# Kernel optimization log

Hardware: AMD Instinct MI355X
Metric: run time of the kernel (lower is better)

The kernel has to match this reference:

```python
import jax, jax.numpy as jnp
import numpy as np

HT_H, HT_W = 512, 512          # Hough accumulator grid
SPHERE_SIZE = 32768            # Gaussian-sphere bins
NUM_VOTES = 1_500_000          # rows in vote_mapping
BATCH, CHANNEL = 2, 64         # channel % 4 == 0 required by the module


def setup_inputs() -> dict:
    key = jax.random.key(0)
    k1, k2, k3, k4 = jax.random.split(key, 4)
    x = jax.random.normal(k1, (BATCH, CHANNEL, HT_H, HT_W), dtype=jnp.float32)
    ht_idx = jax.random.randint(k2, (NUM_VOTES,), 0, HT_H * HT_W, dtype=jnp.int32)
    sphere_idx = jax.random.randint(k3, (NUM_VOTES,), 0, SPHERE_SIZE, dtype=jnp.int32)
    weight = jax.random.uniform(k4, (NUM_VOTES,), dtype=jnp.float32)
    return {"x": x, "ht_idx": ht_idx, "sphere_idx": sphere_idx, "weight": weight}


def reference(x, ht_idx, sphere_idx, weight):
    b, c, h, w = x.shape
    # SPHERE_CUDA.forward: split channels into 4 groups, flatten HT grid
    xf = x.reshape(b * 4, c // 4, h * w)              # [B4, C4, HW]
    # HT2SPHERE: gather each vote's HT cell, scale by vote weight,
    # scatter-add into its sphere bin.
    votes = xf[:, :, ht_idx] * weight                  # [B4, C4, V]
    out = jax.ops.segment_sum(
        jnp.moveaxis(votes, -1, 0), sphere_idx, num_segments=SPHERE_SIZE
    )                                                  # [S, B4, C4]
    out = jnp.moveaxis(out, 0, -1)                     # [B4, C4, S]
    return out.reshape(b, c, SPHERE_SIZE)              # [B, C, S]
```

## Files before the change

### kernel.cpp

```cpp
#include <hip/hip_runtime.h>
#include <stdint.h>


#define S_BINS   32768
#define NBUCKET  1024
#define BINS     32
#define CAP      2048
#define CHUNK    4096
#define HT_BITS  18

__device__ __forceinline__ unsigned bf16_rne(float f) {
    unsigned u = __float_as_uint(f);
    return (u + 0x7FFFu + ((u >> 16) & 1u)) >> 16;
}

__global__ void transpose_x_bf16_kernel(const float* __restrict__ x,
                                        uint32_t* __restrict__ xTb, int HW) {
    __shared__ float tile[64][129];
    const int ht0 = blockIdx.x * 64;
    const int tid = threadIdx.x;
    for (int e = tid; e < 128 * 64; e += 256) {
        const int ch = e >> 6, hl = e & 63;
        tile[hl][ch] = x[(size_t)ch * HW + ht0 + hl];
    }
    __syncthreads();
    for (int e = tid; e < 64 * 64; e += 256) {
        const int hl = e >> 6, cp = e & 63;
        const unsigned lo = bf16_rne(tile[hl][cp]);
        const unsigned hi = bf16_rne(tile[hl][cp + 64]);
        xTb[(size_t)(ht0 + hl) * 64 + cp] = lo | (hi << 16);
    }
}

__global__ void init_kernel(int* __restrict__ cursor, int* __restrict__ spillCnt) {
    const int t = threadIdx.x;
    cursor[t] = t * CAP;
    if (t == 0) *spillCnt = 0;
}

__global__ __launch_bounds__(512) void reorder_kernel(
    const int* __restrict__ ht, const int* __restrict__ sp,
    const float* __restrict__ w, int* __restrict__ cursor,
    uint2* __restrict__ records, uint2* __restrict__ spillRec,
    int* __restrict__ spillBkt, int* __restrict__ spillCnt, int V) {
    __shared__ uint2 rec[CHUNK];
    __shared__ uint16_t bid[CHUNK];
    __shared__ int hist[NBUCKET], start[NBUCKET], cur[NBUCKET], gbase[NBUCKET];
    __shared__ int psum[512];
    const int blk = blockIdx.x, t = threadIdx.x;
    const int base = blk * CHUNK, end = min(V, base + CHUNK), n = end - base;
    hist[2 * t] = 0; hist[2 * t + 1] = 0;
    __syncthreads();
    for (int v = base + t; v < end; v += 512) atomicAdd(&hist[sp[v] >> 5], 1);
    __syncthreads();
    const int l0 = hist[2 * t], l1 = hist[2 * t + 1];
    psum[t] = l0 + l1;
    __syncthreads();
    for (int off = 1; off < 512; off <<= 1) {
        const int add = (t >= off) ? psum[t - off] : 0;
        __syncthreads();
        psum[t] += add;
        __syncthreads();
    }
    int run = (t == 0) ? 0 : psum[t - 1];
    start[2 * t]     = run; cur[2 * t]     = run; run += l0;
    start[2 * t + 1] = run; cur[2 * t + 1] = run;
    if (l0) gbase[2 * t]     = atomicAdd(&cursor[2 * t],     l0);
    if (l1) gbase[2 * t + 1] = atomicAdd(&cursor[2 * t + 1], l1);
    __syncthreads();
    for (int v = base + t; v < end; v += 512) {
        const int s = sp[v];
        const int b = s >> 5, sl = s & 31;
        const int pos = atomicAdd(&cur[b], 1);
        rec[pos] = make_uint2((unsigned)ht[v] | ((unsigned)sl << HT_BITS),
                              __float_as_uint(w[v]));
        bid[pos] = (uint16_t)b;
    }
    __syncthreads();
    for (int i = t; i < n; i += 512) {
        const int b = bid[i];
        const int slot = gbase[b] + (i - start[b]);
        if (slot < (b + 1) * CAP) {
            records[slot] = rec[i];
        } else {
            const int pos = atomicAdd(spillCnt, 1);
            spillRec[pos] = rec[i];
            spillBkt[pos] = b;
        }
    }
}

__global__ __launch_bounds__(512) void accum_kernel(
    const uint32_t* __restrict__ xTb, const uint2* __restrict__ records,
    const int* __restrict__ cursor, float* __restrict__ out) {
    __shared__ uint2 sorted[CAP];
    __shared__ __align__(16) char rawbuf[BINS * 129 * 4];
    __shared__ int hist[BINS], off[BINS + 1], cur[BINS];
    uint2* raw = (uint2*)rawbuf;
    const uint2* xTb2 = (const uint2*)xTb;
    const int bkt = blockIdx.x, t = threadIdx.x;
    const int lane = t & 63, wv = t >> 6;
    const int half = lane >> 5, hl = lane & 31;
    const int n = min(cursor[bkt] - bkt * CAP, CAP);
    const int rbase = bkt * CAP;
    float a[4][4];
#pragma unroll
    for (int i = 0; i < 4; ++i)
#pragma unroll
        for (int j = 0; j < 4; ++j) a[i][j] = 0.f;

    if (t < BINS) hist[t] = 0;
    __syncthreads();
    for (int i = t; i < n; i += 512) {
        const uint2 r = records[rbase + i];
        raw[i] = r;
        atomicAdd(&hist[(r.x >> HT_BITS) & 31], 1);
    }
    __syncthreads();
    if (t == 0) {
        int run = 0;
        for (int j = 0; j < BINS; ++j) { off[j] = run; cur[j] = run; run += hist[j]; }
        off[BINS] = run;
    }
    __syncthreads();
    for (int i = t; i < n; i += 512) {
        const uint2 r = raw[i];
        const int pos = atomicAdd(&cur[(r.x >> HT_BITS) & 31], 1);
        sorted[pos] = r;
    }
    __syncthreads();
#pragma unroll
    for (int bb = 0; bb < 4; ++bb) {
        const int f = wv * 4 + bb;
        const int s0 = off[f], s1 = off[f + 1];
        for (int k = s0; k < s1; k += 16) {
#pragma unroll
            for (int u = 0; u < 8; ++u) {
                const int kk = k + 2 * u + half;
                if (kk < s1) {
                    const uint2 r = sorted[kk];
                    const uint2 g = xTb2[(size_t)(r.x & 0x3FFFF) * 32 + hl];
                    const float wt = __uint_as_float(r.y);
                    a[bb][0] += __uint_as_float(g.x << 16) * wt;
                    a[bb][1] += __uint_as_float(g.x & 0xFFFF0000u) * wt;
                    a[bb][2] += __uint_as_float(g.y << 16) * wt;
                    a[bb][3] += __uint_as_float(g.y & 0xFFFF0000u) * wt;
                }
            }
        }
    }
#pragma unroll
    for (int bb = 0; bb < 4; ++bb)
#pragma unroll
        for (int j = 0; j < 4; ++j)
            a[bb][j] += __shfl_xor(a[bb][j], 32);
    __syncthreads();
    float* epi = (float*)rawbuf;
    if (half == 0) {
#pragma unroll
        for (int bb = 0; bb < 4; ++bb) {
            const int f = wv * 4 + bb;
            epi[f * 129 + 2 * hl]      = a[bb][0];
            epi[f * 129 + 2 * hl + 64] = a[bb][1];
            epi[f * 129 + 2 * hl + 1]  = a[bb][2];
            epi[f * 129 + 2 * hl + 65] = a[bb][3];
        }
    }
    __syncthreads();
    for (int i = t; i < 128 * BINS; i += 512) {
        const int ch = i >> 5, bin = i & 31;
        out[(size_t)ch * S_BINS + bkt * BINS + bin] = epi[bin * 129 + ch];
    }
}

__global__ void spill_kernel(const uint32_t* __restrict__ xTb,
                             const uint2* __restrict__ spillRec,
                             const int* __restrict__ spillBkt,
                             const int* __restrict__ spillCnt,
                             float* __restrict__ out) {
    const int cnt = *spillCnt;
    const long total = (long)cnt * 64;
    for (long u = (long)blockIdx.x * blockDim.x + threadIdx.x; u < total;
         u += (long)gridDim.x * blockDim.x) {
        const int i  = (int)(u >> 6);
        const int cp = (int)(u & 63);
        const uint2 r = spillRec[i];
        const int s = (spillBkt[i] << 5) | ((r.x >> HT_BITS) & 31);
        const uint32_t g = xTb[(size_t)(r.x & 0x3FFFF) * 64 + cp];
        const float wt = __uint_as_float(r.y);
        atomicAdd(&out[(size_t)cp * S_BINS + s],
                  __uint_as_float(g << 16) * wt);
        atomicAdd(&out[(size_t)(cp + 64) * S_BINS + s],
                  __uint_as_float(g & 0xFFFF0000u) * wt);
    }
}

__global__ void direct_kernel(const float* __restrict__ x,
                              const int* __restrict__ ht_idx,
                              const int* __restrict__ sp_idx,
                              const float* __restrict__ weight,
                              float* __restrict__ out, int V, int HW, int S,
                              int CH) {
    const int v = blockIdx.x * 2 + (threadIdx.x >> 7);
    if (v >= V) return;
    const int ch = threadIdx.x & 127;
    if (ch >= CH) return;
    atomicAdd(&out[(size_t)ch * S + sp_idx[v]],
              x[(size_t)ch * HW + ht_idx[v]] * weight[v]);
}

extern "C" void kernel_launch(void* const* d_in, const int* in_sizes, int n_in,
                              void* d_out, int out_size, void* d_ws, size_t ws_size,
                              hipStream_t stream) {
    const float* x  = (const float*)d_in[0];
    const int*   ht = (const int*)d_in[1];
    const int*   sp = (const int*)d_in[2];
    const float* w  = (const float*)d_in[3];
    float* out = (float*)d_out;

    const int HW = 512 * 512;
    const int CH = in_sizes[0] / HW;
    const int S  = out_size / CH;
    const int V  = in_sizes[1];
    const int nblk = (V + CHUNK - 1) / CHUNK;

    const size_t xTb_bytes = (size_t)CH * HW * sizeof(uint16_t);
    const size_t rec_bytes = (size_t)NBUCKET * CAP * sizeof(uint2);
    const size_t spr_bytes = (size_t)V * sizeof(uint2);
    const size_t spb_bytes = (size_t)V * sizeof(int);
    const size_t cur_bytes = (size_t)NBUCKET * sizeof(int);
    const size_t cnt_bytes = 64;
    const size_t need = xTb_bytes + rec_bytes + spr_bytes + spb_bytes +
                        cur_bytes + cnt_bytes;

    if (CH == 128 && S == S_BINS && HW == (1 << HT_BITS) && ws_size >= need) {
        char* p = (char*)d_ws;
        uint32_t* xTb  = (uint32_t*)p;  p += xTb_bytes;
        uint2* records = (uint2*)p;     p += rec_bytes;
        uint2* spillRec= (uint2*)p;     p += spr_bytes;
        int* spillBkt  = (int*)p;       p += spb_bytes;
        int* cursor    = (int*)p;       p += cur_bytes;
        int* spillCnt  = (int*)p;

        init_kernel<<<1, NBUCKET, 0, stream>>>(cursor, spillCnt);
        transpose_x_bf16_kernel<<<HW / 64, 256, 0, stream>>>(x, xTb, HW);
        reorder_kernel<<<nblk, 512, 0, stream>>>(ht, sp, w, cursor, records,
                                                 spillRec, spillBkt, spillCnt, V);
        accum_kernel<<<NBUCKET, 512, 0, stream>>>(xTb, records, cursor, out);
        spill_kernel<<<256, 256, 0, stream>>>(xTb, spillRec, spillBkt, spillCnt,
                                              out);
    } else {
        hipMemsetAsync(out, 0, (size_t)out_size * sizeof(float), stream);
        direct_kernel<<<(V + 1) / 2, 256, 0, stream>>>(x, ht, sp, w, out, V, HW,
                                                       S, CH);
    }
}
```

Baseline: 316.9 us.

## Widen accum gathers to 16-byte loads, fold spill handling into accum

The accum kernel now has each lane gather a uint4 (8 bf16 channels), with 16 lanes covering a row instead of 32, and reduces the partial sums across the wave with two shuffles. The separate spill kernel is removed. Each accum block instead scans the spill list for records belonging to its bucket and adds them with shared-memory atomics before writing out. The reorder kernel also caches sphere indices in LDS rather than reading them from global memory twice. The changes trade extra registers and a per-block scan of the spill list for fewer global loads and one less launch.

After: 314.8 us. No clear change (-0.6%).

```diff
diff --git a/kernel.cpp b/kernel.cpp
--- a/kernel.cpp
+++ b/kernel.cpp
@@ -45,13 +45,18 @@
     int* __restrict__ spillBkt, int* __restrict__ spillCnt, int V) {
     __shared__ uint2 rec[CHUNK];
     __shared__ uint16_t bid[CHUNK];
+    __shared__ uint16_t sval[CHUNK];
     __shared__ int hist[NBUCKET], start[NBUCKET], cur[NBUCKET], gbase[NBUCKET];
     __shared__ int psum[512];
     const int blk = blockIdx.x, t = threadIdx.x;
     const int base = blk * CHUNK, end = min(V, base + CHUNK), n = end - base;
     hist[2 * t] = 0; hist[2 * t + 1] = 0;
     __syncthreads();
-    for (int v = base + t; v < end; v += 512) atomicAdd(&hist[sp[v] >> 5], 1);
+    for (int v = base + t; v < end; v += 512) {
+        const int s = sp[v];
+        sval[v - base] = (uint16_t)s;
+        atomicAdd(&hist[s >> 5], 1);
+    }
     __syncthreads();
     const int l0 = hist[2 * t], l1 = hist[2 * t + 1];
     psum[t] = l0 + l1;
@@ -69,7 +74,7 @@
     if (l1) gbase[2 * t + 1] = atomicAdd(&cursor[2 * t + 1], l1);
     __syncthreads();
     for (int v = base + t; v < end; v += 512) {
-        const int s = sp[v];
+        const int s = (int)sval[v - base];
         const int b = s >> 5, sl = s & 31;
         const int pos = atomicAdd(&cur[b], 1);
         rec[pos] = make_uint2((unsigned)ht[v] | ((unsigned)sl << HT_BITS),
@@ -92,22 +97,24 @@
 
 __global__ __launch_bounds__(512) void accum_kernel(
     const uint32_t* __restrict__ xTb, const uint2* __restrict__ records,
-    const int* __restrict__ cursor, float* __restrict__ out) {
+    const int* __restrict__ cursor, const uint2* __restrict__ spillRec,
+    const int* __restrict__ spillBkt, const int* __restrict__ spillCnt,
+    float* __restrict__ out) {
     __shared__ uint2 sorted[CAP];
     __shared__ __align__(16) char rawbuf[BINS * 129 * 4];
     __shared__ int hist[BINS], off[BINS + 1], cur[BINS];
     uint2* raw = (uint2*)rawbuf;
-    const uint2* xTb2 = (const uint2*)xTb;
+    const uint4* xTb4 = (const uint4*)xTb;
     const int bkt = blockIdx.x, t = threadIdx.x;
     const int lane = t & 63, wv = t >> 6;
-    const int half = lane >> 5, hl = lane & 31;
+    const int q = lane >> 4, ql = lane & 15;
     const int n = min(cursor[bkt] - bkt * CAP, CAP);
     const int rbase = bkt * CAP;
-    float a[4][4];
+    float a[4][8];
 #pragma unroll
     for (int i = 0; i < 4; ++i)
 #pragma unroll
-        for (int j = 0; j < 4; ++j) a[i][j] = 0.f;
+        for (int j = 0; j < 8; ++j) a[i][j] = 0.f;
 
     if (t < BINS) hist[t] = 0;
     __syncthreads();
@@ -133,18 +140,23 @@
     for (int bb = 0; bb < 4; ++bb) {
         const int f = wv * 4 + bb;
         const int s0 = off[f], s1 = off[f + 1];
+#pragma unroll 1
         for (int k = s0; k < s1; k += 16) {
 #pragma unroll
-            for (int u = 0; u < 8; ++u) {
-                const int kk = k + 2 * u + half;
+            for (int u = 0; u < 4; ++u) {
+                const int kk = k + 4 * u + q;
                 if (kk < s1) {
                     const uint2 r = sorted[kk];
-                    const uint2 g = xTb2[(size_t)(r.x & 0x3FFFF) * 32 + hl];
+                    const uint4 g = xTb4[(size_t)(r.x & 0x3FFFF) * 16 + ql];
                     const float wt = __uint_as_float(r.y);
-                    a[bb][0] += __uint_as_float(g.x << 16) * wt;
-                    a[bb][1] += __uint_as_float(g.x & 0xFFFF0000u) * wt;
-                    a[bb][2] += __uint_as_float(g.y << 16) * wt;
-                    a[bb][3] += __uint_as_float(g.y & 0xFFFF0000u) * wt;
+                    a[bb][0] += __uint_as_float(g.x << 16)          * wt;
+                    a[bb][1] += __uint_as_float(g.x & 0xFFFF0000u)  * wt;
+                    a[bb][2] += __uint_as_float(g.y << 16)          * wt;
+                    a[bb][3] += __uint_as_float(g.y & 0xFFFF0000u)  * wt;
+                    a[bb][4] += __uint_as_float(g.z << 16)          * wt;
+                    a[bb][5] += __uint_as_float(g.z & 0xFFFF0000u)  * wt;
+                    a[bb][6] += __uint_as_float(g.w << 16)          * wt;
+                    a[bb][7] += __uint_as_float(g.w & 0xFFFF0000u)  * wt;
                 }
             }
         }
@@ -152,46 +164,52 @@
 #pragma unroll
     for (int bb = 0; bb < 4; ++bb)
 #pragma unroll
-        for (int j = 0; j < 4; ++j)
+        for (int j = 0; j < 8; ++j) {
+            a[bb][j] += __shfl_xor(a[bb][j], 16);
             a[bb][j] += __shfl_xor(a[bb][j], 32);
+        }
     __syncthreads();
     float* epi = (float*)rawbuf;
-    if (half == 0) {
+    if (lane < 16) {
 #pragma unroll
         for (int bb = 0; bb < 4; ++bb) {
             const int f = wv * 4 + bb;
-            epi[f * 129 + 2 * hl]      = a[bb][0];
-            epi[f * 129 + 2 * hl + 64] = a[bb][1];
-            epi[f * 129 + 2 * hl + 1]  = a[bb][2];
-            epi[f * 129 + 2 * hl + 65] = a[bb][3];
-        }
-    }
-    __syncthreads();
+            epi[f * 129 + 4 * ql]      = a[bb][0];
+            epi[f * 129 + 4 * ql + 64] = a[bb][1];
+            epi[f * 129 + 4 * ql + 1]  = a[bb][2];
+            epi[f * 129 + 4 * ql + 65] = a[bb][3];
+            epi[f * 129 + 4 * ql + 2]  = a[bb][4];
+            epi[f * 129 + 4 * ql + 66] = a[bb][5];
+            epi[f * 129 + 4 * ql + 3]  = a[bb][6];
+            epi[f * 129 + 4 * ql + 67] = a[bb][7];
+        }
+    }
+    __syncthreads();
+    const int cnt = *spillCnt;
+    if (cnt > 0) {
+        const uint2* xTb2 = (const uint2*)xTb;
+        const int hl = lane & 31;
+        for (int i = t >> 5; i < cnt; i += 16) {
+            if (spillBkt[i] == bkt) {
+                const uint2 r = spillRec[i];
+                const int f = (r.x >> HT_BITS) & 31;
+                const uint2 g = xTb2[(size_t)(r.x & 0x3FFFF) * 32 + hl];
+                const float wt = __uint_as_float(r.y);
+                atomicAdd(&epi[f * 129 + 2 * hl],
+                          __uint_as_float(g.x << 16) * wt);
+                atomicAdd(&epi[f * 129 + 2 * hl + 64],
+                          __uint_as_float(g.x & 0xFFFF0000u) * wt);
+                atomicAdd(&epi[f * 129 + 2 * hl + 1],
+                          __uint_as_float(g.y << 16) * wt);
+                atomicAdd(&epi[f * 129 + 2 * hl + 65],
+                          __uint_as_float(g.y & 0xFFFF0000u) * wt);
+            }
+        }
+        __syncthreads();
+    }
     for (int i = t; i < 128 * BINS; i += 512) {
         const int ch = i >> 5, bin = i & 31;
         out[(size_t)ch * S_BINS + bkt * BINS + bin] = epi[bin * 129 + ch];
-    }
-}
-
-__global__ void spill_kernel(const uint32_t* __restrict__ xTb,
-                             const uint2* __restrict__ spillRec,
-                             const int* __restrict__ spillBkt,
-                             const int* __restrict__ spillCnt,
-                             float* __restrict__ out) {
-    const int cnt = *spillCnt;
-    const long total = (long)cnt * 64;
-    for (long u = (long)blockIdx.x * blockDim.x + threadIdx.x; u < total;
-         u += (long)gridDim.x * blockDim.x) {
-        const int i  = (int)(u >> 6);
-        const int cp = (int)(u & 63);
-        const uint2 r = spillRec[i];
-        const int s = (spillBkt[i] << 5) | ((r.x >> HT_BITS) & 31);
-        const uint32_t g = xTb[(size_t)(r.x & 0x3FFFF) * 64 + cp];
-        const float wt = __uint_as_float(r.y);
-        atomicAdd(&out[(size_t)cp * S_BINS + s],
-                  __uint_as_float(g << 16) * wt);
-        atomicAdd(&out[(size_t)(cp + 64) * S_BINS + s],
-                  __uint_as_float(g & 0xFFFF0000u) * wt);
     }
 }
 
@@ -246,9 +264,9 @@
         transpose_x_bf16_kernel<<<HW / 64, 256, 0, stream>>>(x, xTb, HW);
         reorder_kernel<<<nblk, 512, 0, stream>>>(ht, sp, w, cursor, records,
                                                  spillRec, spillBkt, spillCnt, V);
-        accum_kernel<<<NBUCKET, 512, 0, stream>>>(xTb, records, cursor, out);
-        spill_kernel<<<256, 256, 0, stream>>>(xTb, spillRec, spillBkt, spillCnt,
-                                              out);
+        accum_kernel<<<NBUCKET, 512, 0, stream>>>(xTb, records, cursor,
+                                                  spillRec, spillBkt, spillCnt,
+                                                  out);
     } else {
         hipMemsetAsync(out, 0, (size_t)out_size * sizeof(float), stream);
         direct_kernel<<<(V + 1) / 2, 256, 0, stream>>>(x, ht, sp, w, out, V, HW,
```
